# Performance work log

Measured on AMD Instinct MI355X. Metric: run time of the kernel, lower is better.

## Reference

```python
import jax, jax.numpy as jnp
import numpy as np

N = 8192
IN_F = 256
OUT_F = 64
ALPHA = 0.2  # LeakyReLU negative slope
NEG_INF = -9e15


def setup_inputs() -> dict:
    key = jax.random.key(0)
    k1, k2, k3, k4 = jax.random.split(key, 4)
    input_h = jax.random.normal(k1, (N, IN_F), dtype=jnp.float32)
    # xavier_normal with gain=1.414 ~ std = 1.414*sqrt(2/(fan_in+fan_out))
    W = jax.random.normal(k2, (IN_F, OUT_F), dtype=jnp.float32) * (1.414 * np.sqrt(2.0 / (IN_F + OUT_F)))
    a = jax.random.normal(k3, (2 * OUT_F, 1), dtype=jnp.float32) * (1.414 * np.sqrt(2.0 / (2 * OUT_F + 1)))
    adj = jax.random.randint(k4, (N, N), 0, 2).astype(jnp.int32)
    return {"input_h": input_h, "adj": adj, "W": W, "a": a}


def reference(input_h, adj, W, a):
    # h = X @ W : [N, OUT_F]
    h = input_h @ W
    # Pairwise concat score: a^T [h_i || h_j] == (h_i @ a1) + (h_j @ a2)
    a1 = a[:OUT_F]   # [OUT_F, 1]
    a2 = a[OUT_F:]   # [OUT_F, 1]
    f1 = h @ a1      # [N, 1] -> contribution of source node i
    f2 = h @ a2      # [N, 1] -> contribution of target node j
    e = jax.nn.leaky_relu(f1 + f2.T, negative_slope=ALPHA)  # [N, N]
    # Masked softmax over neighbors (adj > 0), dropout is identity in eval mode
    attention = jax.nn.softmax(jnp.where(adj > 0, e, NEG_INF), axis=-1)
    h_prime = attention @ h  # [N, OUT_F]
    # concat=True -> ELU activation
    return jax.nn.elu(h_prime)
```

## Files before the change

kernel.cpp:

```cpp
#include <hip/hip_runtime.h>
#include <hip/hip_bf16.h>


using short8 = __attribute__((ext_vector_type(8))) short;
using f32x4  = __attribute__((ext_vector_type(4))) float;

#define NN     8192
#define INF_   256
#define OUTF   64
#define LR_A   0.2f
#define LOG2E  1.4426950408889634f
#define ROWS   16
#define BPAD   1040

__device__ __forceinline__ unsigned short f2bf_rne(float x) {
  unsigned int u = __float_as_uint(x);
  u += 0x7FFFu + ((u >> 16) & 1u);
  return (unsigned short)(u >> 16);
}

__global__ __launch_bounds__(256) void gat_pre(
    const float* __restrict__ input, const float* __restrict__ W,
    const float* __restrict__ a, unsigned short* __restrict__ hp,
    float* __restrict__ f1, float* __restrict__ f2) {
  __shared__ float WT[OUTF][260];
  int tid = threadIdx.x;
  for (int idx = tid; idx < INF_ * OUTF; idx += 256) {
    int c = idx >> 6, f = idx & 63;
    WT[f][c] = W[idx];
  }
  __syncthreads();
  int w = tid >> 6, l = tid & 63;
  int i0 = blockIdx.x * 16 + w * 4;
  const float4* r0 = (const float4*)(input + (long)(i0 + 0) * INF_);
  const float4* r1 = (const float4*)(input + (long)(i0 + 1) * INF_);
  const float4* r2 = (const float4*)(input + (long)(i0 + 2) * INF_);
  const float4* r3 = (const float4*)(input + (long)(i0 + 3) * INF_);
  float h0 = 0.f, h1 = 0.f, h2 = 0.f, h3 = 0.f;
#pragma unroll 4
  for (int c4 = 0; c4 < INF_ / 4; ++c4) {
    float4 wv = *(const float4*)&WT[l][c4 * 4];
    float4 v0 = r0[c4], v1 = r1[c4], v2 = r2[c4], v3 = r3[c4];
    h0 = fmaf(v0.x, wv.x, h0); h0 = fmaf(v0.y, wv.y, h0);
    h0 = fmaf(v0.z, wv.z, h0); h0 = fmaf(v0.w, wv.w, h0);
    h1 = fmaf(v1.x, wv.x, h1); h1 = fmaf(v1.y, wv.y, h1);
    h1 = fmaf(v1.z, wv.z, h1); h1 = fmaf(v1.w, wv.w, h1);
    h2 = fmaf(v2.x, wv.x, h2); h2 = fmaf(v2.y, wv.y, h2);
    h2 = fmaf(v2.z, wv.z, h2); h2 = fmaf(v2.w, wv.w, h2);
    h3 = fmaf(v3.x, wv.x, h3); h3 = fmaf(v3.y, wv.y, h3);
    h3 = fmaf(v3.z, wv.z, h3); h3 = fmaf(v3.w, wv.w, h3);
  }
  float a1k = a[l], a2k = a[OUTF + l];
  float hh[4] = {h0, h1, h2, h3};
#pragma unroll
  for (int r = 0; r < 4; ++r) {
    int i = i0 + r;
    float t1 = hh[r] * a1k, t2 = hh[r] * a2k;
#pragma unroll
    for (int off = 32; off; off >>= 1) {
      t1 += __shfl_xor(t1, off);
      t2 += __shfl_xor(t2, off);
    }
    int gran = (((i >> 5) * 4) + (l >> 4)) * 64 + ((i >> 3) & 3) * 16 + (l & 15);
    hp[(long)gran * 8 + (i & 7)] = f2bf_rne(hh[r]);
    if (l == 0) { f1[i] = t1 * LOG2E; f2[i] = t2 * LOG2E; }
  }
}

__global__ __launch_bounds__(256, 3) void gat_main(
    const int* __restrict__ adj, const unsigned short* __restrict__ hp,
    const float* __restrict__ f1, const float* __restrict__ f2,
    float* __restrict__ out) {
  __shared__ __align__(16) unsigned char bitsL[ROWS * BPAD];
  __shared__ float f2s[NN];
  __shared__ float ssum[4][ROWS];
  __shared__ float f1s[ROWS], shifts[ROWS], red[4];
  int tid = threadIdx.x;
  int w = tid >> 6, l = tid & 63;
  int i0 = blockIdx.x * ROWS;

  float fm = -1e30f;
  for (int jj = tid * 4; jj < NN; jj += 1024) {
    float4 v = *(const float4*)(f2 + jj);
    *(float4*)&f2s[jj] = v;
    fm = fmaxf(fm, fmaxf(fmaxf(v.x, v.y), fmaxf(v.z, v.w)));
  }
#pragma unroll
  for (int off = 32; off; off >>= 1) fm = fmaxf(fm, __shfl_xor(fm, off));
  if (l == 0) red[w] = fm;
  __syncthreads();
  if (tid == 0) red[0] = fmaxf(fmaxf(red[0], red[1]), fmaxf(red[2], red[3]));
  __syncthreads();
  float Fmax = red[0];
  if (tid < ROWS) {
    float v = f1[i0 + tid];
    f1s[tid] = v;
    float s = v + Fmax;
    shifts[tid] = fmaxf(s, LR_A * s);
  }

#pragma unroll
  for (int r = 0; r < 4; ++r) {
    int rr = w * 4 + r;
    const int4* rowp = (const int4*)(adj + (long)(i0 + rr) * NN) + l * 2;
    unsigned char* brow = bitsL + rr * BPAD + l;
#pragma unroll 4
    for (int c = 0; c < 16; ++c) {
      int4 a = rowp[c * 128], b = rowp[c * 128 + 1];
      unsigned bt = (a.x > 0) | ((a.y > 0) << 1) | ((a.z > 0) << 2) |
                    ((a.w > 0) << 3) | ((b.x > 0) << 4) | ((b.y > 0) << 5) |
                    ((b.z > 0) << 6) | ((b.w > 0) << 7);
      brow[c * 64] = (unsigned char)bt;
    }
  }
  __syncthreads();

  int q = l & 15, g = l >> 4;
  float f1r = f1s[q], sh = shifts[q];
  float u1 = f1r - sh, u2 = LR_A * f1r - sh;
  f32x4 acc0 = {0.f, 0.f, 0.f, 0.f}, acc1 = acc0, acc2 = acc0, acc3 = acc0;
  float srow = 0.f;

  const unsigned char* bq = bitsL + q * BPAD + w * 256 + g;
  const float* f2w = f2s + w * 2048 + g * 8;
  const unsigned short* hpw = hp + (long)w * 64 * 2048 + l * 8;

  short8 hA[4], hB[4];
  auto load_hp = [&](short8* d, int t) {
    const unsigned short* p = hpw + (long)t * 2048;
    d[0] = *(const short8*)(p);
    d[1] = *(const short8*)(p + 512);
    d[2] = *(const short8*)(p + 1024);
    d[3] = *(const short8*)(p + 1536);
  };
  auto compute = [&](int t, const short8* H) {
    unsigned bt = bq[t * 4];
    const float* fb = f2w + t * 32;
    float4 F0 = *(const float4*)fb, F1 = *(const float4*)(fb + 4);
    float fa[8] = {F0.x, F0.y, F0.z, F0.w, F1.x, F1.y, F1.z, F1.w};
    union { short8 v; unsigned short u[8]; } pa;
    float ps = 0.f;
#pragma unroll
    for (int e = 0; e < 8; ++e) {
      float arg = fmaxf(u1 + fa[e], fmaf(LR_A, fa[e], u2));
      float pe = (bt & (1u << e)) ? exp2f(arg) : 0.f;
      ps += pe;
      pa.u[e] = f2bf_rne(pe);
    }
    srow += ps;
    acc0 = __builtin_amdgcn_mfma_f32_16x16x32_bf16(pa.v, H[0], acc0, 0, 0, 0);
    acc1 = __builtin_amdgcn_mfma_f32_16x16x32_bf16(pa.v, H[1], acc1, 0, 0, 0);
    acc2 = __builtin_amdgcn_mfma_f32_16x16x32_bf16(pa.v, H[2], acc2, 0, 0, 0);
    acc3 = __builtin_amdgcn_mfma_f32_16x16x32_bf16(pa.v, H[3], acc3, 0, 0, 0);
  };

  load_hp(hA, 0);
  for (int tt = 0; tt < 64; tt += 2) {
    load_hp(hB, tt + 1);
    compute(tt, hA);
    if (tt + 2 < 64) load_hp(hA, tt + 2);
    compute(tt + 1, hB);
  }

  srow += __shfl_xor(srow, 16);
  srow += __shfl_xor(srow, 32);

  __syncthreads();
  if (l < ROWS) ssum[w][l] = srow;
  float* accs = (float*)bitsL;
#pragma unroll
  for (int r = 0; r < 4; ++r) {
    accs[(w * ROWS + g * 4 + r) * OUTF + 0 * 16 + q] = acc0[r];
    accs[(w * ROWS + g * 4 + r) * OUTF + 1 * 16 + q] = acc1[r];
    accs[(w * ROWS + g * 4 + r) * OUTF + 2 * 16 + q] = acc2[r];
    accs[(w * ROWS + g * 4 + r) * OUTF + 3 * 16 + q] = acc3[r];
  }
  __syncthreads();

  for (int idx = tid; idx < ROWS * OUTF; idx += 256) {
    int m = idx >> 6, n = idx & 63;
    float num = 0.f, den = 0.f;
#pragma unroll
    for (int ww = 0; ww < 4; ++ww) {
      num += accs[(ww * ROWS + m) * OUTF + n];
      den += ssum[ww][m];
    }
    float v = num / den;
    out[(long)(i0 + m) * OUTF + n] = v > 0.f ? v : expm1f(v);
  }
}

extern "C" void kernel_launch(void* const* d_in, const int* in_sizes, int n_in,
                              void* d_out, int out_size, void* d_ws, size_t ws_size,
                              hipStream_t stream) {
  const float* input = (const float*)d_in[0];
  const int*   adj   = (const int*)d_in[1];
  const float* W     = (const float*)d_in[2];
  const float* a     = (const float*)d_in[3];
  float* out = (float*)d_out;
  char* ws = (char*)d_ws;
  unsigned short* hp = (unsigned short*)ws;
  float* f1 = (float*)(ws + (1 << 20));
  float* f2 = (float*)(ws + (1 << 20) + (32 << 10));
  (void)in_sizes; (void)n_in; (void)out_size; (void)ws_size;

  gat_pre<<<512, 256, 0, stream>>>(input, W, a, hp, f1, f2);
  gat_main<<<512, 256, 0, stream>>>(adj, hp, f1, f2, out);
}
```

Baseline: 106.4 us.

## Split attention columns across two blocks with partial sums and finalize kernel

Splits the column range of each row block into two halves using a second grid dimension. This doubles the number of blocks, halves shared memory per block (allowing occupancy 4), and writes partial numerators and denominators that a new small kernel combines and passes through ELU. Adjacency loads are also switched to nontemporal loads. In exchange it adds an extra kernel launch and a round trip of the partial results through global memory.

```diff
diff --git a/kernel.cpp b/kernel.cpp
--- a/kernel.cpp
+++ b/kernel.cpp
@@ -4,6 +4,7 @@
 
 using short8 = __attribute__((ext_vector_type(8))) short;
 using f32x4  = __attribute__((ext_vector_type(4))) float;
+using i32x4  = __attribute__((ext_vector_type(4))) int;
 
 #define NN     8192
 #define INF_   256
@@ -11,7 +12,8 @@
 #define LR_A   0.2f
 #define LOG2E  1.4426950408889634f
 #define ROWS   16
-#define BPAD   1040
+#define HCOLS  4096
+#define BPAD   528
 
 __device__ __forceinline__ unsigned short f2bf_rne(float x) {
   unsigned int u = __float_as_uint(x);
@@ -67,24 +69,26 @@
   }
 }
 
-__global__ __launch_bounds__(256, 3) void gat_main(
+__global__ __launch_bounds__(256, 4) void gat_main(
     const int* __restrict__ adj, const unsigned short* __restrict__ hp,
     const float* __restrict__ f1, const float* __restrict__ f2,
-    float* __restrict__ out) {
+    float* __restrict__ numP, float* __restrict__ denP) {
   __shared__ __align__(16) unsigned char bitsL[ROWS * BPAD];
-  __shared__ float f2s[NN];
+  __shared__ __align__(16) float f2s[HCOLS];
   __shared__ float ssum[4][ROWS];
   __shared__ float f1s[ROWS], shifts[ROWS], red[4];
   int tid = threadIdx.x;
   int w = tid >> 6, l = tid & 63;
   int i0 = blockIdx.x * ROWS;
+  int ch = blockIdx.y;
 
   float fm = -1e30f;
   for (int jj = tid * 4; jj < NN; jj += 1024) {
     float4 v = *(const float4*)(f2 + jj);
-    *(float4*)&f2s[jj] = v;
     fm = fmaxf(fm, fmaxf(fmaxf(v.x, v.y), fmaxf(v.z, v.w)));
   }
+  for (int jj = tid * 4; jj < HCOLS; jj += 1024)
+    *(float4*)&f2s[jj] = *(const float4*)(f2 + ch * HCOLS + jj);
 #pragma unroll
   for (int off = 32; off; off >>= 1) fm = fmaxf(fm, __shfl_xor(fm, off));
   if (l == 0) red[w] = fm;
@@ -102,14 +106,16 @@
 #pragma unroll
   for (int r = 0; r < 4; ++r) {
     int rr = w * 4 + r;
-    const int4* rowp = (const int4*)(adj + (long)(i0 + rr) * NN) + l * 2;
+    const i32x4* rowp = (const i32x4*)(adj + (long)(i0 + rr) * NN + ch * HCOLS)
+                        + l * 2;
     unsigned char* brow = bitsL + rr * BPAD + l;
-#pragma unroll 4
-    for (int c = 0; c < 16; ++c) {
-      int4 a = rowp[c * 128], b = rowp[c * 128 + 1];
-      unsigned bt = (a.x > 0) | ((a.y > 0) << 1) | ((a.z > 0) << 2) |
-                    ((a.w > 0) << 3) | ((b.x > 0) << 4) | ((b.y > 0) << 5) |
-                    ((b.z > 0) << 6) | ((b.w > 0) << 7);
+#pragma unroll
+    for (int c = 0; c < 8; ++c) {
+      i32x4 a = __builtin_nontemporal_load(rowp + c * 128);
+      i32x4 b = __builtin_nontemporal_load(rowp + c * 128 + 1);
+      unsigned bt = (a[0] > 0) | ((a[1] > 0) << 1) | ((a[2] > 0) << 2) |
+                    ((a[3] > 0) << 3) | ((b[0] > 0) << 4) | ((b[1] > 0) << 5) |
+                    ((b[2] > 0) << 6) | ((b[3] > 0) << 7);
       brow[c * 64] = (unsigned char)bt;
     }
   }
@@ -121,9 +127,9 @@
   f32x4 acc0 = {0.f, 0.f, 0.f, 0.f}, acc1 = acc0, acc2 = acc0, acc3 = acc0;
   float srow = 0.f;
 
-  const unsigned char* bq = bitsL + q * BPAD + w * 256 + g;
-  const float* f2w = f2s + w * 2048 + g * 8;
-  const unsigned short* hpw = hp + (long)w * 64 * 2048 + l * 8;
+  const unsigned char* bq = bitsL + q * BPAD + w * 128 + g;
+  const float* f2w = f2s + w * 1024 + g * 8;
+  const unsigned short* hpw = hp + (long)(ch * 128 + w * 32) * 2048 + l * 8;
 
   short8 hA[4], hB[4];
   auto load_hp = [&](short8* d, int t) {
@@ -155,10 +161,10 @@
   };
 
   load_hp(hA, 0);
-  for (int tt = 0; tt < 64; tt += 2) {
+  for (int tt = 0; tt < 32; tt += 2) {
     load_hp(hB, tt + 1);
     compute(tt, hA);
-    if (tt + 2 < 64) load_hp(hA, tt + 2);
+    if (tt + 2 < 32) load_hp(hA, tt + 2);
     compute(tt + 1, hB);
   }
 
@@ -167,7 +173,7 @@
 
   __syncthreads();
   if (l < ROWS) ssum[w][l] = srow;
-  float* accs = (float*)bitsL;
+  float* accs = f2s;
 #pragma unroll
   for (int r = 0; r < 4; ++r) {
     accs[(w * ROWS + g * 4 + r) * OUTF + 0 * 16 + q] = acc0[r];
@@ -185,9 +191,20 @@
       num += accs[(ww * ROWS + m) * OUTF + n];
       den += ssum[ww][m];
     }
-    float v = num / den;
-    out[(long)(i0 + m) * OUTF + n] = v > 0.f ? v : expm1f(v);
-  }
+    numP[((long)ch * NN + i0 + m) * OUTF + n] = num;
+    if (n == 0) denP[(long)ch * NN + i0 + m] = den;
+  }
+}
+
+__global__ __launch_bounds__(256) void gat_fin(
+    const float* __restrict__ numP, const float* __restrict__ denP,
+    float* __restrict__ out) {
+  int gid = blockIdx.x * 256 + threadIdx.x;
+  int row = gid >> 6;
+  float num = numP[gid] + numP[(long)NN * OUTF + gid];
+  float den = denP[row] + denP[NN + row];
+  float v = num / den;
+  out[gid] = v > 0.f ? v : expm1f(v);
 }
 
 extern "C" void kernel_launch(void* const* d_in, const int* in_sizes, int n_in,
@@ -200,10 +217,13 @@
   float* out = (float*)d_out;
   char* ws = (char*)d_ws;
   unsigned short* hp = (unsigned short*)ws;
-  float* f1 = (float*)(ws + (1 << 20));
-  float* f2 = (float*)(ws + (1 << 20) + (32 << 10));
+  float* f1   = (float*)(ws + (1 << 20));
+  float* f2   = (float*)(ws + (1 << 20) + (32 << 10));
+  float* numP = (float*)(ws + (1 << 20) + (64 << 10));
+  float* denP = (float*)(ws + (1 << 20) + (64 << 10) + (4 << 20));
   (void)in_sizes; (void)n_in; (void)out_size; (void)ws_size;
 
   gat_pre<<<512, 256, 0, stream>>>(input, W, a, hp, f1, f2);
-  gat_main<<<512, 256, 0, stream>>>(adj, hp, f1, f2, out);
-}
+  gat_main<<<dim3(512, 2), 256, 0, stream>>>(adj, hp, f1, f2, numP, denP);
+  gat_fin<<<NN * OUTF / 256, 256, 0, stream>>>(numP, denP, out);
+}
```

After: 111.6 us. 1.05x slower.
